# Optimization experiments

Hardware: AMD Instinct MI355X
Metric: run time of the kernel (lower is better)

Reference implementation:

```python
import jax, jax.numpy as jnp
import numpy as np

TEMP = 0.2
M, K, B = 8192, 128, 100


def setup_inputs() -> dict:
    key = jax.random.key(0)
    k1, k2, k3 = jax.random.split(key, 3)
    f = jax.random.normal(k1, (M, K), dtype=jnp.float32)
    features = f / jnp.linalg.norm(f, axis=1, keepdims=True)
    p = jax.random.normal(k2, (B, K), dtype=jnp.float32)
    protos = p / jnp.linalg.norm(p, axis=1, keepdims=True)
    labels = jax.random.randint(k3, (M,), 0, 2 * B, dtype=jnp.int32)
    proto_labels = jnp.arange(B, dtype=jnp.int32)
    return {"features": features, "labels": labels, "protos": protos, "proto_labels": proto_labels}


def reference(features, labels, protos, proto_labels):
    m = features.shape[0]
    dt = features.dtype
    # base = samples whose label appears among prototype labels
    base = (labels[None, :] == proto_labels[:, None]).any(axis=0)  # [M] bool
    novel = ~base
    nf = novel.astype(dt)
    bf = base.astype(dt)

    S = jnp.matmul(features, features.T) / TEMP          # [M, M] sample-sample logits
    P = jnp.matmul(features, protos.T) / TEMP            # [M, B] sample-proto logits

    # novel-novel pair mask: both novel, off-diagonal (fill_diagonal_(0))
    pair = nf[:, None] * nf[None, :] * (1.0 - jnp.eye(m, dtype=dt))  # [M, M]
    expS = jnp.exp(S)

    # --- novel loss (note: original adds RAW ni_pk.sum, not exp -- faithful) ---
    exp_sum = (expS * pair).sum(axis=1)                  # sum_{j novel, j!=i} exp(S_ij)
    denom = exp_sum + P.sum(axis=1)                      # + raw proto logit sum
    safe_den = jnp.where(novel, denom, 1.0)
    cnt = pair.sum(axis=1)                               # novel_label_mask is all-True 1D -> just pair count
    safe_cnt = jnp.where(cnt > 0, cnt, 1.0)
    # sum_j pair_ij * (S_ij - log(den_i)) = (S*pair).sum - log(den)*cnt
    num = (S * pair).sum(axis=1) - jnp.log(safe_den) * cnt
    loss_novel = (-(num / safe_cnt) * nf).sum()

    # --- base loss ---
    safe_lab = jnp.where(base, labels, 0)
    bi_pi = jnp.take_along_axis(P, safe_lab[:, None], axis=1)[:, 0]  # P[i, labels[i]]
    exp_nk = (expS * nf[None, :]).sum(axis=1)            # sum over novel columns
    exp_pk = jnp.exp(P).sum(axis=1)
    loss_base = (-(bi_pi - jnp.log(exp_nk + exp_pk)) * bf).sum()

    return (loss_novel + loss_base) / m
```

## Files before the change

### kernel.cpp

```cpp
#include <hip/hip_runtime.h>
#include <stdint.h>


#define M_TOT 8192
#define K_DIM 128
#define B_PRO 100
#define INV_T 5.0f
#define C_SCALE 7.2134752044448170f
#define LN2    0.6931471805599453f
#define RT    256
#define NT    (M_TOT / RT)
#define NPAIR (NT * (NT - 1) / 2)
#define NBLK  (NT + NPAIR)
#define BS    136
#define PB    112

#if __has_builtin(__builtin_amdgcn_exp2f)
#define EXP2(x) __builtin_amdgcn_exp2f(x)
#else
#define EXP2(x) __expf((x) * 0.6931471805599453f)
#endif

typedef __attribute__((ext_vector_type(8))) short  short8;
typedef __attribute__((ext_vector_type(4))) float  floatx4;

__device__ __forceinline__ float bf2f(unsigned short u) {
    union { unsigned int i; float f; } v; v.i = ((unsigned int)u) << 16; return v.f;
}
__device__ __forceinline__ unsigned short f2bf(float x) {
    __bf16 b = (__bf16)x;
    return __builtin_bit_cast(unsigned short, b);
}
__device__ __forceinline__ short8 pack8(float4 a, float4 b) {
    short8 r;
    r[0] = (short)f2bf(a.x); r[1] = (short)f2bf(a.y);
    r[2] = (short)f2bf(a.z); r[3] = (short)f2bf(a.w);
    r[4] = (short)f2bf(b.x); r[5] = (short)f2bf(b.y);
    r[6] = (short)f2bf(b.z); r[7] = (short)f2bf(b.w);
    return r;
}

template<bool DIAG>
__device__ __forceinline__ void sym_body(
        int a, int b, int R0, int C0,
        const float* __restrict__ feat, const int* __restrict__ labels,
        const float* __restrict__ protos, const int* __restrict__ plabels,
        float* __restrict__ rowE,
        int* __restrict__ nfpart, int* __restrict__ nf,
        float* __restrict__ Psum, float* __restrict__ expPsum,
        float* __restrict__ PLab, float* __restrict__ gpart,
        unsigned short* ldsB, float (*colE)[256],
        float* novR, float* novC, int* plabL, int* labRow, float* redD) {
    const int tid = threadIdx.x;
    const int wv = tid >> 6, lane = tid & 63;
    const int quad = lane >> 4, cq = lane & 15;

    if (tid < B_PRO) plabL[tid] = plabels[tid];

    short8 afr[2][4];
    #pragma unroll
    for (int mt = 0; mt < 2; ++mt)
        #pragma unroll
        for (int ks = 0; ks < 4; ++ks) {
            const float* s = feat + (size_t)(R0 + wv * 32 + mt * 16 + cq) * K_DIM
                             + ks * 32 + quad * 8;
            float4 x = ((const float4*)s)[0];
            float4 y = ((const float4*)s)[1];
            afr[mt][ks] = pack8(x, y);
        }
    __syncthreads();

    {
        const int g = (tid < 256) ? (R0 + tid) : (C0 + (tid - 256));
        const int lbl = labels[g];
        int m = 0;
        #pragma unroll 4
        for (int j = 0; j < B_PRO; ++j) m |= (plabL[j] == lbl);
        const float nv = m ? 0.f : 1.f;
        if (tid < 256) { novR[tid] = nv; labRow[tid] = lbl; }
        else novC[tid - 256] = nv;
    }
    __syncthreads();

    float nmR[2][4];
    #pragma unroll
    for (int mt = 0; mt < 2; ++mt)
        #pragma unroll
        for (int r = 0; r < 4; ++r)
            nmR[mt][r] = novR[wv * 32 + mt * 16 + quad * 4 + r];
    float nmcA[16];
    #pragma unroll
    for (int c2 = 0; c2 < 16; ++c2)
        nmcA[c2] = novC[c2 * 16 + cq];

    float accE[2][4];
    #pragma unroll
    for (int mt = 0; mt < 2; ++mt)
        #pragma unroll
        for (int r = 0; r < 4; ++r) accE[mt][r] = 0.f;

    float g_acc = 0.f;

    const int rbase = R0 + wv * 32 + quad * 4;

    #pragma unroll 1
    for (int half = 0; half < 2; ++half) {
        for (int e = tid; e < 2048; e += 512) {
            const int col = e >> 4, sg = e & 15;
            const float* s = feat + (size_t)(C0 + half * 128 + col) * K_DIM + sg * 8;
            float4 x = ((const float4*)s)[0];
            float4 y = ((const float4*)s)[1];
            ushort4 o0 = make_ushort4(f2bf(x.x*C_SCALE), f2bf(x.y*C_SCALE),
                                      f2bf(x.z*C_SCALE), f2bf(x.w*C_SCALE));
            ushort4 o1 = make_ushort4(f2bf(y.x*C_SCALE), f2bf(y.y*C_SCALE),
                                      f2bf(y.z*C_SCALE), f2bf(y.w*C_SCALE));
            *(ushort4*)&ldsB[col * BS + sg * 8]     = o0;
            *(ushort4*)&ldsB[col * BS + sg * 8 + 4] = o1;
        }
        __syncthreads();

        #pragma unroll 2
        for (int ct8 = 0; ct8 < 8; ++ct8) {
            const int ct = half * 8 + ct8;
            const unsigned short* bp = &ldsB[(ct8 * 16 + cq) * BS + quad * 8];
            short8 b0 = *(const short8*)(bp);
            short8 b1 = *(const short8*)(bp + 32);
            short8 b2 = *(const short8*)(bp + 64);
            short8 b3 = *(const short8*)(bp + 96);

            floatx4 D0 = (floatx4){0.f, 0.f, 0.f, 0.f};
            floatx4 D1 = (floatx4){0.f, 0.f, 0.f, 0.f};
            D0 = __builtin_amdgcn_mfma_f32_16x16x32_bf16(afr[0][0], b0, D0, 0, 0, 0);
            D0 = __builtin_amdgcn_mfma_f32_16x16x32_bf16(afr[0][1], b1, D0, 0, 0, 0);
            D0 = __builtin_amdgcn_mfma_f32_16x16x32_bf16(afr[0][2], b2, D0, 0, 0, 0);
            D0 = __builtin_amdgcn_mfma_f32_16x16x32_bf16(afr[0][3], b3, D0, 0, 0, 0);
            D1 = __builtin_amdgcn_mfma_f32_16x16x32_bf16(afr[1][0], b0, D1, 0, 0, 0);
            D1 = __builtin_amdgcn_mfma_f32_16x16x32_bf16(afr[1][1], b1, D1, 0, 0, 0);
            D1 = __builtin_amdgcn_mfma_f32_16x16x32_bf16(afr[1][2], b2, D1, 0, 0, 0);
            D1 = __builtin_amdgcn_mfma_f32_16x16x32_bf16(afr[1][3], b3, D1, 0, 0, 0);

            const float nmc = nmcA[ct];
            float cpE = 0.f;
            #pragma unroll
            for (int r = 0; r < 4; ++r) {
                float e0 = EXP2(D0[r]), e1 = EXP2(D1[r]);
                if (DIAG) {
                    const int colg = C0 + ct * 16 + cq;
                    if (rbase + r == colg) e0 = 0.f;
                    if (rbase + 16 + r == colg) e1 = 0.f;
                }
                accE[0][r] += e0 * nmc;  cpE += e0 * nmR[0][r];
                accE[1][r] += e1 * nmc;  cpE += e1 * nmR[1][r];
            }
            cpE += __shfl_xor(cpE, 16); cpE += __shfl_xor(cpE, 32);
            if (quad == 0) colE[wv][ct * 16 + cq] = cpE;
        }

        if (DIAG && tid < 128) {
            float s = 0.f;
            #pragma unroll 4
            for (int c2 = 0; c2 < 128; ++c2)
                s += novC[half * 128 + c2] * bf2f(ldsB[c2 * BS + tid]);
            g_acc += s;
        }
        __syncthreads();
    }

    #pragma unroll
    for (int mt = 0; mt < 2; ++mt)
        #pragma unroll
        for (int r = 0; r < 4; ++r) {
            float e = accE[mt][r];
            e += __shfl_xor(e, 1); e += __shfl_xor(e, 2);
            e += __shfl_xor(e, 4); e += __shfl_xor(e, 8);
            accE[mt][r] = e;
        }
    if (cq == 0) {
        const size_t slotR = (size_t)b * M_TOT;
        #pragma unroll
        for (int mt = 0; mt < 2; ++mt)
            #pragma unroll
            for (int r = 0; r < 4; ++r) {
                const int rowg = R0 + wv * 32 + mt * 16 + quad * 4 + r;
                rowE[slotR + rowg] = accE[mt][r];
            }
    }

    if (!DIAG) {
        if (tid < 256) {
            float ce = 0.f;
            #pragma unroll
            for (int w = 0; w < 8; ++w) ce += colE[w][tid];
            rowE[(size_t)a * M_TOT + C0 + tid] = ce;
        }
    } else {
        if (tid < 128) gpart[a * 128 + tid] = g_acc;
        {
            float nvv = (tid < 256) ? novR[tid] : 0.f;
            for (int off = 1; off < 64; off <<= 1) nvv += __shfl_xor(nvv, off);
            if (lane == 0) redD[wv] = nvv;
        }
        if (tid < 256) nf[R0 + tid] = (int)novR[tid];

        for (int idx = tid; idx < 3200; idx += 512) {
            const int pr = idx >> 5, sg = idx & 31;
            float4 v = ((const float4*)protos)[idx];
            *(ushort4*)&ldsB[pr * BS + sg * 4] =
                make_ushort4(f2bf(v.x), f2bf(v.y), f2bf(v.z), f2bf(v.w));
        }
        for (int idx = tid; idx < 384; idx += 512) {
            const int pr = B_PRO + (idx >> 5), sg = idx & 31;
            *(ushort4*)&ldsB[pr * BS + sg * 4] = make_ushort4(0, 0, 0, 0);
        }
        __syncthreads();

        if (tid == 0) {
            float c = 0.f;
            #pragma unroll
            for (int w = 0; w < 8; ++w) c += redD[w];
            nfpart[a] = (int)c;
        }

        float ps2[2][4], es2[2][4], pl2[2][4];
        #pragma unroll
        for (int mt = 0; mt < 2; ++mt)
            #pragma unroll
            for (int r = 0; r < 4; ++r) { ps2[mt][r]=0.f; es2[mt][r]=0.f; pl2[mt][r]=0.f; }

        #pragma unroll 1
        for (int g = 0; g < 7; ++g) {
            const unsigned short* bp = &ldsB[(g * 16 + cq) * BS + quad * 8];
            short8 b0 = *(const short8*)(bp);
            short8 b1 = *(const short8*)(bp + 32);
            short8 b2 = *(const short8*)(bp + 64);
            short8 b3 = *(const short8*)(bp + 96);
            floatx4 E0 = (floatx4){0.f, 0.f, 0.f, 0.f};
            floatx4 E1 = (floatx4){0.f, 0.f, 0.f, 0.f};
            E0 = __builtin_amdgcn_mfma_f32_16x16x32_bf16(afr[0][0], b0, E0, 0, 0, 0);
            E0 = __builtin_amdgcn_mfma_f32_16x16x32_bf16(afr[0][1], b1, E0, 0, 0, 0);
            E0 = __builtin_amdgcn_mfma_f32_16x16x32_bf16(afr[0][2], b2, E0, 0, 0, 0);
            E0 = __builtin_amdgcn_mfma_f32_16x16x32_bf16(afr[0][3], b3, E0, 0, 0, 0);
            E1 = __builtin_amdgcn_mfma_f32_16x16x32_bf16(afr[1][0], b0, E1, 0, 0, 0);
            E1 = __builtin_amdgcn_mfma_f32_16x16x32_bf16(afr[1][1], b1, E1, 0, 0, 0);
            E1 = __builtin_amdgcn_mfma_f32_16x16x32_bf16(afr[1][2], b2, E1, 0, 0, 0);
            E1 = __builtin_amdgcn_mfma_f32_16x16x32_bf16(afr[1][3], b3, E1, 0, 0, 0);
            const int bcol = g * 16 + cq;
            if (bcol < B_PRO) {
                #pragma unroll
                for (int r = 0; r < 4; ++r) {
                    const float Pv0 = E0[r] * INV_T;
                    ps2[0][r] += Pv0; es2[0][r] += __expf(Pv0);
                    if (bcol == labRow[wv * 32 + quad * 4 + r]) pl2[0][r] += Pv0;
                    const float Pv1 = E1[r] * INV_T;
                    ps2[1][r] += Pv1; es2[1][r] += __expf(Pv1);
                    if (bcol == labRow[wv * 32 + 16 + quad * 4 + r]) pl2[1][r] += Pv1;
                }
            }
        }
        #pragma unroll
        for (int mt = 0; mt < 2; ++mt)
            #pragma unroll
            for (int r = 0; r < 4; ++r) {
                float p = ps2[mt][r], e = es2[mt][r], l = pl2[mt][r];
                p += __shfl_xor(p, 1); p += __shfl_xor(p, 2);
                p += __shfl_xor(p, 4); p += __shfl_xor(p, 8);
                e += __shfl_xor(e, 1); e += __shfl_xor(e, 2);
                e += __shfl_xor(e, 4); e += __shfl_xor(e, 8);
                l += __shfl_xor(l, 1); l += __shfl_xor(l, 2);
                l += __shfl_xor(l, 4); l += __shfl_xor(l, 8);
                if (cq == 0) {
                    const int rowg = R0 + wv * 32 + mt * 16 + quad * 4 + r;
                    Psum[rowg] = p; expPsum[rowg] = e; PLab[rowg] = l;
                }
            }
    }
}

__global__ __launch_bounds__(512, 4) void k_sym(
        const float* __restrict__ feat, const int* __restrict__ labels,
        const float* __restrict__ protos, const int* __restrict__ plabels,
        float* __restrict__ rowE,
        int* __restrict__ nfpart, int* __restrict__ nf,
        float* __restrict__ Psum, float* __restrict__ expPsum,
        float* __restrict__ PLab, float* __restrict__ gpart,
        float* __restrict__ out) {
    __shared__ unsigned short ldsB[128 * BS];
    __shared__ float colE[8][256];
    __shared__ float novR[256];
    __shared__ float novC[256];
    __shared__ int plabL[B_PRO];
    __shared__ int labRow[256];
    __shared__ float redD[8];

    if (blockIdx.x == 0 && threadIdx.x == 0) out[0] = 0.f;

    const int id = blockIdx.x;
    if (id < NT) {
        sym_body<true>(id, id, id * RT, id * RT,
                       feat, labels, protos, plabels, rowE,
                       nfpart, nf, Psum, expPsum, PLab, gpart,
                       ldsB, colE, novR, novC, plabL, labRow, redD);
    } else {
        const int p = id - NT;
        int aa = 0, rem = p;
        while (rem >= NT - 1 - aa) { rem -= (NT - 1 - aa); ++aa; }
        const int bb2 = aa + 1 + rem;
        sym_body<false>(aa, bb2, aa * RT, bb2 * RT,
                        feat, labels, protos, plabels, rowE,
                        nfpart, nf, Psum, expPsum, PLab, gpart,
                        ldsB, colE, novR, novC, plabL, labRow, redD);
    }
}

__global__ __launch_bounds__(128) void k_final(
        const float* __restrict__ feat,
        const float* __restrict__ rowE,
        const float* __restrict__ Psum, const float* __restrict__ expPsum,
        const float* __restrict__ PLab, const int* __restrict__ nf,
        const int* __restrict__ nfpart, const float* __restrict__ gpart,
        float* __restrict__ out) {
    __shared__ float g[128];
    __shared__ int shNn;
    __shared__ float red[2];
    const int tid = threadIdx.x;
    const int i = blockIdx.x * 128 + tid;

    {
        float s = 0.f;
        #pragma unroll 4
        for (int a2 = 0; a2 < 32; ++a2) s += gpart[a2 * 128 + tid];
        g[tid] = s;
    }
    if (tid < 32) {
        int c = nfpart[tid];
        for (int off = 1; off < 32; off <<= 1) c += __shfl_xor(c, off);
        if (tid == 0) shNn = c;
    }
    __syncthreads();

    float e0 = 0.f, e1 = 0.f, e2 = 0.f, e3 = 0.f;
    #pragma unroll
    for (int s = 0; s < 8; ++s) {
        e0 += rowE[(size_t)(4 * s + 0) * M_TOT + i];
        e1 += rowE[(size_t)(4 * s + 1) * M_TOT + i];
        e2 += rowE[(size_t)(4 * s + 2) * M_TOT + i];
        e3 += rowE[(size_t)(4 * s + 3) * M_TOT + i];
    }
    const float ep = (e0 + e1) + (e2 + e3);

    const float* fr = feat + (size_t)i * K_DIM;
    float sZ = 0.f, dd = 0.f;
    #pragma unroll 8
    for (int k4 = 0; k4 < 32; ++k4) {
        float4 v = ((const float4*)fr)[k4];
        const float fb0 = bf2f(f2bf(v.x)), fc0 = bf2f(f2bf(v.x * C_SCALE));
        const float fb1 = bf2f(f2bf(v.y)), fc1 = bf2f(f2bf(v.y * C_SCALE));
        const float fb2 = bf2f(f2bf(v.z)), fc2 = bf2f(f2bf(v.z * C_SCALE));
        const float fb3 = bf2f(f2bf(v.w)), fc3 = bf2f(f2bf(v.w * C_SCALE));
        const float* gv = &g[k4 * 4];
        sZ += fb0 * gv[0]; dd += fb0 * fc0;
        sZ += fb1 * gv[1]; dd += fb1 * fc1;
        sZ += fb2 * gv[2]; dd += fb2 * fc2;
        sZ += fb3 * gv[3]; dd += fb3 * fc3;
    }

    const int Nn = shNn;
    float contrib;
    if (nf[i]) {
        const float cnt = (float)(Nn - 1);
        const float denom = ep + Psum[i];
        const float sp = sZ - dd;
        const float num = sp * LN2 - logf(denom) * cnt;
        const float sc = cnt > 0.f ? cnt : 1.f;
        contrib = -(num / sc);
    } else {
        contrib = -(PLab[i] - logf(ep + expPsum[i]));
    }
    for (int off = 1; off < 64; off <<= 1) contrib += __shfl_xor(contrib, off);
    if ((tid & 63) == 0) red[tid >> 6] = contrib;
    __syncthreads();
    if (tid == 0) atomicAdd(out, (red[0] + red[1]) * (1.0f / (float)M_TOT));
}

extern "C" void kernel_launch(void* const* d_in, const int* in_sizes, int n_in,
                              void* d_out, int out_size, void* d_ws, size_t ws_size,
                              hipStream_t stream) {
    const float* feat    = (const float*)d_in[0];
    const int*   labels  = (const int*)d_in[1];
    const float* protos  = (const float*)d_in[2];
    const int*   plabels = (const int*)d_in[3];
    float* out = (float*)d_out;

    char* ws = (char*)d_ws;
    float* rowE    = (float*)ws;
    int*   nfpart  = (int*)(ws + 1048576);
    int*   nf      = (int*)(ws + 1052672);
    float* Psum    = (float*)(ws + 1085440);
    float* expPsum = (float*)(ws + 1118208);
    float* PLab    = (float*)(ws + 1150976);
    float* gpart   = (float*)(ws + 1183744);

    k_sym<<<NBLK, 512, 0, stream>>>(feat, labels, protos, plabels,
                                    rowE, nfpart, nf,
                                    Psum, expPsum, PLab, gpart, out);
    k_final<<<64, 128, 0, stream>>>(feat, rowE, Psum, expPsum, PLab,
                                    nf, nfpart, gpart, out);
}
```

Baseline: 101.2 us.

## Fuse final reduction into main kernel using last-blocks ticket counter

Removes the separate k_final launch. Each block of the symmetric tile kernel takes a ticket from a global atomic counter. The last 64 ticket holders spin until every block has arrived, then each finishes a 128-row slice of the per-row loss, with 4 threads per row combined by shuffles. This saves a kernel launch and the gap between the two kernels. In exchange it adds a global atomic per block, spin-waiting tail blocks, and it relies on a monotonically increasing counter across calls.

```diff
diff --git a/kernel.cpp b/kernel.cpp
--- a/kernel.cpp
+++ b/kernel.cpp
@@ -12,6 +12,7 @@
 #define NT    (M_TOT / RT)
 #define NPAIR (NT * (NT - 1) / 2)
 #define NBLK  (NT + NPAIR)
+#define NTAIL 64
 #define BS    136
 #define PB    112
 
@@ -23,6 +24,8 @@
 
 typedef __attribute__((ext_vector_type(8))) short  short8;
 typedef __attribute__((ext_vector_type(4))) float  floatx4;
+
+__device__ int g_counter;
 
 __device__ __forceinline__ float bf2f(unsigned short u) {
     union { unsigned int i; float f; } v; v.i = ((unsigned int)u) << 16; return v.f;
@@ -276,7 +279,7 @@
     }
 }
 
-__global__ __launch_bounds__(512, 4) void k_sym(
+__global__ __launch_bounds__(512, 4) void k_fused(
         const float* __restrict__ feat, const int* __restrict__ labels,
         const float* __restrict__ protos, const int* __restrict__ plabels,
         float* __restrict__ rowE,
@@ -291,8 +294,11 @@
     __shared__ int plabL[B_PRO];
     __shared__ int labRow[256];
     __shared__ float redD[8];
-
-    if (blockIdx.x == 0 && threadIdx.x == 0) out[0] = 0.f;
+    __shared__ int ticket;
+    __shared__ int shNn;
+
+    const int tid = threadIdx.x;
+    if (blockIdx.x == 0 && tid == 0) out[0] = 0.f;
 
     const int id = blockIdx.x;
     if (id < NT) {
@@ -310,26 +316,29 @@
                         nfpart, nf, Psum, expPsum, PLab, gpart,
                         ldsB, colE, novR, novC, plabL, labRow, redD);
     }
-}
-
-__global__ __launch_bounds__(128) void k_final(
-        const float* __restrict__ feat,
-        const float* __restrict__ rowE,
-        const float* __restrict__ Psum, const float* __restrict__ expPsum,
-        const float* __restrict__ PLab, const int* __restrict__ nf,
-        const int* __restrict__ nfpart, const float* __restrict__ gpart,
-        float* __restrict__ out) {
-    __shared__ float g[128];
-    __shared__ int shNn;
-    __shared__ float red[2];
-    const int tid = threadIdx.x;
-    const int i = blockIdx.x * 128 + tid;
-
-    {
+
+    __threadfence();
+    __syncthreads();
+    if (tid == 0) ticket = atomicAdd(&g_counter, 1);
+    __syncthreads();
+    const int t = ticket;
+    const int base = (t / NBLK) * NBLK;
+    const int rank = t - base;
+    if (rank < NBLK - NTAIL) return;
+    const int slice = rank - (NBLK - NTAIL);
+
+    if (tid == 0) {
+        const int target = base + NBLK;
+        while (atomicAdd(&g_counter, 0) < target) __builtin_amdgcn_s_sleep(2);
+    }
+    __syncthreads();
+    __threadfence();
+
+    if (tid < 128) {
         float s = 0.f;
         #pragma unroll 4
         for (int a2 = 0; a2 < 32; ++a2) s += gpart[a2 * 128 + tid];
-        g[tid] = s;
+        novC[tid] = s;
     }
     if (tid < 32) {
         int c = nfpart[tid];
@@ -338,48 +347,55 @@
     }
     __syncthreads();
 
-    float e0 = 0.f, e1 = 0.f, e2 = 0.f, e3 = 0.f;
-    #pragma unroll
-    for (int s = 0; s < 8; ++s) {
-        e0 += rowE[(size_t)(4 * s + 0) * M_TOT + i];
-        e1 += rowE[(size_t)(4 * s + 1) * M_TOT + i];
-        e2 += rowE[(size_t)(4 * s + 2) * M_TOT + i];
-        e3 += rowE[(size_t)(4 * s + 3) * M_TOT + i];
-    }
-    const float ep = (e0 + e1) + (e2 + e3);
+    const int rp = tid >> 2, u = tid & 3;
+    const int i = slice * 128 + rp;
+
+    float ep = 0.f;
+    #pragma unroll
+    for (int s = u; s < 32; s += 4) ep += rowE[(size_t)s * M_TOT + i];
 
     const float* fr = feat + (size_t)i * K_DIM;
     float sZ = 0.f, dd = 0.f;
-    #pragma unroll 8
-    for (int k4 = 0; k4 < 32; ++k4) {
+    #pragma unroll
+    for (int k4 = u * 8; k4 < u * 8 + 8; ++k4) {
         float4 v = ((const float4*)fr)[k4];
         const float fb0 = bf2f(f2bf(v.x)), fc0 = bf2f(f2bf(v.x * C_SCALE));
         const float fb1 = bf2f(f2bf(v.y)), fc1 = bf2f(f2bf(v.y * C_SCALE));
         const float fb2 = bf2f(f2bf(v.z)), fc2 = bf2f(f2bf(v.z * C_SCALE));
         const float fb3 = bf2f(f2bf(v.w)), fc3 = bf2f(f2bf(v.w * C_SCALE));
-        const float* gv = &g[k4 * 4];
+        const float* gv = &novC[k4 * 4];
         sZ += fb0 * gv[0]; dd += fb0 * fc0;
         sZ += fb1 * gv[1]; dd += fb1 * fc1;
         sZ += fb2 * gv[2]; dd += fb2 * fc2;
         sZ += fb3 * gv[3]; dd += fb3 * fc3;
     }
-
-    const int Nn = shNn;
-    float contrib;
-    if (nf[i]) {
-        const float cnt = (float)(Nn - 1);
-        const float denom = ep + Psum[i];
-        const float sp = sZ - dd;
-        const float num = sp * LN2 - logf(denom) * cnt;
-        const float sc = cnt > 0.f ? cnt : 1.f;
-        contrib = -(num / sc);
-    } else {
-        contrib = -(PLab[i] - logf(ep + expPsum[i]));
+    ep += __shfl_xor(ep, 1); ep += __shfl_xor(ep, 2);
+    sZ += __shfl_xor(sZ, 1); sZ += __shfl_xor(sZ, 2);
+    dd += __shfl_xor(dd, 1); dd += __shfl_xor(dd, 2);
+
+    float contrib = 0.f;
+    if (u == 0) {
+        const int Nn = shNn;
+        if (nf[i]) {
+            const float cnt = (float)(Nn - 1);
+            const float denom = ep + Psum[i];
+            const float sp = sZ - dd;
+            const float num = sp * LN2 - logf(denom) * cnt;
+            const float sc = cnt > 0.f ? cnt : 1.f;
+            contrib = -(num / sc);
+        } else {
+            contrib = -(PLab[i] - logf(ep + expPsum[i]));
+        }
     }
     for (int off = 1; off < 64; off <<= 1) contrib += __shfl_xor(contrib, off);
-    if ((tid & 63) == 0) red[tid >> 6] = contrib;
-    __syncthreads();
-    if (tid == 0) atomicAdd(out, (red[0] + red[1]) * (1.0f / (float)M_TOT));
+    if ((tid & 63) == 0) redD[tid >> 6] = contrib;
+    __syncthreads();
+    if (tid == 0) {
+        float s = 0.f;
+        #pragma unroll
+        for (int w = 0; w < 8; ++w) s += redD[w];
+        atomicAdd(out, s * (1.0f / (float)M_TOT));
+    }
 }
 
 extern "C" void kernel_launch(void* const* d_in, const int* in_sizes, int n_in,
@@ -400,9 +416,7 @@
     float* PLab    = (float*)(ws + 1150976);
     float* gpart   = (float*)(ws + 1183744);
 
-    k_sym<<<NBLK, 512, 0, stream>>>(feat, labels, protos, plabels,
-                                    rowE, nfpart, nf,
-                                    Psum, expPsum, PLab, gpart, out);
-    k_final<<<64, 128, 0, stream>>>(feat, rowE, Psum, expPsum, PLab,
-                                    nf, nfpart, gpart, out);
-}
+    k_fused<<<NBLK, 512, 0, stream>>>(feat, labels, protos, plabels,
+                                      rowE, nfpart, nf,
+                                      Psum, expPsum, PLab, gpart, out);
+}
```

New measurement: 198.5 us. 1.96x slower.
